# Kernel optimization log

Hardware: AMD Instinct MI355X
Metric: run time of the kernel (lower is better)

Reference implementation:

```python
import jax, jax.numpy as jnp
import numpy as np

B, N, D, E = 64, 128, 64, 131072  # graphs, nodes/graph, d_model, edges


def setup_inputs() -> dict:
    key = jax.random.key(0)
    ks = jax.random.split(key, 7)
    x = jax.random.normal(ks[0], (B * N, D), jnp.float32)
    # sorted batch assignment: exactly N nodes per graph
    batch = jnp.repeat(jnp.arange(B, dtype=jnp.int32), N)
    # intra-graph random edges
    eb = jax.random.randint(ks[1], (E,), 0, B)
    ls = jax.random.randint(ks[2], (E,), 0, N)
    ld = jax.random.randint(ks[3], (E,), 0, N)
    edge_index = jnp.stack([eb * N + ls, eb * N + ld], axis=0)
    edge_attr = jax.random.normal(ks[4], (E, D), jnp.float32)
    virtual_x_weight = jax.random.normal(ks[5], (1, D), jnp.float32) * 0.02
    virtual_edge_attr_weight = jax.random.normal(ks[6], (1, D), jnp.float32) * 0.02
    return {
        "x": x,
        "edge_attr": edge_attr,
        "virtual_x_weight": virtual_x_weight,
        "virtual_edge_attr_weight": virtual_edge_attr_weight,
        "batch": batch,
        "edge_index": edge_index,
        "num_graphs": B,
        "max_nodes": N,
    }


def reference(x, edge_attr, virtual_x_weight, virtual_edge_attr_weight,
              batch, edge_index, num_graphs, max_nodes):
    b, n = num_graphs, max_nodes
    total, d = x.shape
    # per-graph node counts and start offsets (to_dense_batch bookkeeping)
    counts = jax.ops.segment_sum(jnp.ones(total, jnp.int32), batch, num_segments=b)
    starts = jnp.cumsum(counts) - counts              # exclusive prefix sum
    pos = jnp.arange(total) - starts[batch]           # local node position in graph

    # to_dense_batch + virtual-node row 0 (scatter directly into padded tensor)
    x_with_vn = jnp.zeros((b, n + 1, d), x.dtype).at[batch, pos + 1].set(x)
    x_with_vn = x_with_vn.at[:, 0, :].set(virtual_x_weight[0])
    mask = jnp.zeros((b, n), bool).at[batch, pos].set(True)

    # to_dense_adj (duplicate edges sum) scattered directly at +1 offsets
    src, dst = edge_index[0], edge_index[1]
    eb = batch[src]
    ls = src - starts[eb] + 1
    ld = dst - starts[eb] + 1
    adj = jnp.zeros((b, n + 1, n + 1, d), edge_attr.dtype).at[eb, ls, ld].add(edge_attr)
    ve = virtual_edge_attr_weight[0]
    adj = adj.at[:, 0, 1:, :].set(ve)
    adj = adj.at[:, 1:, 0, :].set(ve)
    return x_with_vn, adj, mask
```

## Files before the change

### kernel.cpp

```cpp
#include <hip/hip_runtime.h>
#include <stdint.h>

#define NB 64
#define NN 128
#define ND 64
#define NE 131072
#define NP1 129

#define X_ELEMS   (NB * NP1 * ND)
#define ADJ_ELEMS (NB * NP1 * NP1 * ND)
#define MASK_ELEMS (NB * NN)
#define TOTAL_ELEMS (X_ELEMS + ADJ_ELEMS + MASK_ELEMS)

#define NCELLS (NB * NN * NN)
#define CNT_WORDS (NCELLS / 4)
#define WS_REQ ((size_t)CNT_WORDS * 4)


__global__ __launch_bounds__(256) void zero_cnt_kernel(unsigned int* __restrict__ cnt) {
  cnt[blockIdx.x * 256u + threadIdx.x] = 0u;
}

__global__ __launch_bounds__(256) void count_kernel(
    const int* __restrict__ ei, unsigned int* __restrict__ cnt) {
  unsigned int e = blockIdx.x * 256u + threadIdx.x;
  unsigned int src = (unsigned int)ei[e];
  unsigned int dst = (unsigned int)ei[NE + e];
  unsigned int cell = (src << 7) | (dst & 127u);
  atomicAdd(&cnt[cell >> 2], 1u << ((cell & 3u) << 3));
}

__global__ __launch_bounds__(256) void fill_kernel(
    const float* __restrict__ x, const float* __restrict__ vxw,
    const float* __restrict__ vew, float* __restrict__ out) {
  unsigned int base = (blockIdx.x * 256u + threadIdx.x) * 4u;
  float4 r;
  if (base < X_ELEMS) {
    unsigned int d = base & 63u;
    unsigned int rowflat = base >> 6;
    unsigned int row = rowflat % 129u;
    if (row == 0u) r = *(const float4*)(vxw + d);
    else r = *(const float4*)(x + ((((rowflat / 129u) << 7) + row - 1u) << 6) + d);
  } else if (base < X_ELEMS + ADJ_ELEMS) {
    unsigned int rel = base - X_ELEMS;
    unsigned int d = rel & 63u;
    unsigned int rc = rel >> 6;
    unsigned int col = rc % 129u;
    unsigned int row = (rc / 129u) % 129u;
    if ((row == 0u) != (col == 0u)) r = *(const float4*)(vew + d);
    else r = make_float4(0.f, 0.f, 0.f, 0.f);
  } else {
    r = make_float4(1.f, 1.f, 1.f, 1.f);
  }
  *(float4*)(out + base) = r;
}

template <int HYBRID>
__global__ __launch_bounds__(256) void scatter_kernel(
    const float* __restrict__ ea, const int* __restrict__ ei,
    const unsigned int* __restrict__ cnt, float* __restrict__ out) {
  unsigned int t = blockIdx.x * 256u + threadIdx.x;
  unsigned int e = t >> 6, lane = t & 63u;

  unsigned int src = (unsigned int)ei[e];
  unsigned int dst = (unsigned int)ei[NE + e];
  unsigned int eb = src >> 7;
  unsigned int ls = (src & 127u) + 1u;
  unsigned int ld = (dst & 127u) + 1u;
  unsigned int dstIdx = (unsigned int)X_ELEMS +
      (((eb * 129u + ls) * 129u + ld) << 6) + lane;
  float v = ea[(e << 6) + lane];

  if (HYBRID) {
    unsigned int cell = (src << 7) | (dst & 127u);
    unsigned int c = (cnt[cell >> 2] >> ((cell & 3u) << 3)) & 255u;
    if (c == 1u) { out[dstIdx] = v; return; }
  }
  atomicAdd(out + dstIdx, v);
}

extern "C" void kernel_launch(void* const* d_in, const int* in_sizes, int n_in,
                              void* d_out, int out_size, void* d_ws, size_t ws_size,
                              hipStream_t stream) {
  const float* x   = (const float*)d_in[0];
  const float* ea  = (const float*)d_in[1];
  const float* vxw = (const float*)d_in[2];
  const float* vew = (const float*)d_in[3];
  const int* ei = (const int*)d_in[5];
  float* out = (float*)d_out;

  if (ws_size >= WS_REQ) {
    unsigned int* cnt = (unsigned int*)d_ws;
    zero_cnt_kernel<<<CNT_WORDS / 256u, 256, 0, stream>>>(cnt);
    count_kernel<<<NE / 256u, 256, 0, stream>>>(ei, cnt);
    fill_kernel<<<TOTAL_ELEMS / 4u / 256u, 256, 0, stream>>>(x, vxw, vew, out);
    scatter_kernel<1><<<NE * 64u / 256u, 256, 0, stream>>>(ea, ei, cnt, out);
  } else {
    fill_kernel<<<TOTAL_ELEMS / 4u / 256u, 256, 0, stream>>>(x, vxw, vew, out);
    scatter_kernel<0><<<NE * 64u / 256u, 256, 0, stream>>>(ea, ei, nullptr, out);
  }
}
```

Baseline: 85.92 us.

## Replace fill-then-scatter with per-row edge lists gathered during dense build

Adds a binning pass that records each edge's id and destination column in a fixed-capacity per-source-row list alongside the per-cell counts. The dense adjacency is then built in a single pass: each nonzero cell scans its row list and sums the matching edge features, so the separate scatter pass and its second write over the output go away. The cost is a linear scan of up to 96 list entries per nonzero cell, plus random gather reads of edge features. Rows with more than 96 edges would be silently truncated.

Result: slower. 185.2 us (+115.5%).

```diff
diff --git a/kernel.cpp b/kernel.cpp
--- a/kernel.cpp
+++ b/kernel.cpp
@@ -14,20 +14,79 @@
 
 #define NCELLS (NB * NN * NN)
 #define CNT_WORDS (NCELLS / 4)
-#define WS_REQ ((size_t)CNT_WORDS * 4)
+#define NROWS (NB * NN)
+#define ROWCAP 96
+#define LIST_OFF_W (CNT_WORDS + NROWS)
+#define ZERO_WORDS (CNT_WORDS + NROWS)
+#define WS_WORDS (LIST_OFF_W + NROWS * ROWCAP)
+#define WS_REQ ((size_t)WS_WORDS * 4)
 
 
-__global__ __launch_bounds__(256) void zero_cnt_kernel(unsigned int* __restrict__ cnt) {
-  cnt[blockIdx.x * 256u + threadIdx.x] = 0u;
+__global__ __launch_bounds__(256) void zero_kernel(unsigned int* __restrict__ ws) {
+  ws[blockIdx.x * 256u + threadIdx.x] = 0u;
 }
 
-__global__ __launch_bounds__(256) void count_kernel(
-    const int* __restrict__ ei, unsigned int* __restrict__ cnt) {
+__global__ __launch_bounds__(256) void bin_kernel(
+    const int* __restrict__ ei, unsigned int* __restrict__ ws) {
   unsigned int e = blockIdx.x * 256u + threadIdx.x;
   unsigned int src = (unsigned int)ei[e];
   unsigned int dst = (unsigned int)ei[NE + e];
   unsigned int cell = (src << 7) | (dst & 127u);
-  atomicAdd(&cnt[cell >> 2], 1u << ((cell & 3u) << 3));
+  atomicAdd(&ws[cell >> 2], 1u << ((cell & 3u) << 3));
+  unsigned int idx = atomicAdd(&ws[CNT_WORDS + src], 1u);
+  if (idx < ROWCAP)
+    ws[LIST_OFF_W + src * ROWCAP + idx] = (e << 8) | ((dst & 127u) + 1u);
+}
+
+__global__ __launch_bounds__(256) void build_kernel(
+    const float* __restrict__ x, const float* __restrict__ vxw,
+    const float* __restrict__ vew, const float* __restrict__ ea,
+    const unsigned int* __restrict__ ws, float* __restrict__ out) {
+  unsigned int base = (blockIdx.x * 256u + threadIdx.x) * 4u;
+  float4 v;
+
+  if (base < X_ELEMS) {
+    unsigned int d = base & 63u;
+    unsigned int rowflat = base >> 6;
+    unsigned int row = rowflat % 129u;
+    if (row == 0u) v = *(const float4*)(vxw + d);
+    else v = *(const float4*)(x + ((((rowflat / 129u) << 7) + row - 1u) << 6) + d);
+  } else if (base < X_ELEMS + ADJ_ELEMS) {
+    unsigned int rel = base - X_ELEMS;
+    unsigned int d = rel & 63u;
+    unsigned int rc = rel >> 6;
+    unsigned int col = rc % 129u;
+    unsigned int t = rc / 129u;
+    unsigned int row = t % 129u;
+    unsigned int b = t / 129u;
+    if (row != 0u && col != 0u) {
+      unsigned int src  = (b << 7) + row - 1u;
+      unsigned int cell = (src << 7) | (col - 1u);
+      unsigned int n = (ws[cell >> 2] >> ((cell & 3u) << 3)) & 255u;
+      v = make_float4(0.f, 0.f, 0.f, 0.f);
+      if (n != 0u) {
+        unsigned int m = ws[CNT_WORDS + src]; if (m > ROWCAP) m = ROWCAP;
+        const unsigned int* lst = ws + LIST_OFF_W + src * ROWCAP;
+        unsigned int found = 0u;
+        for (unsigned int k = 0u; k < m; ++k) {
+          unsigned int u = lst[k];
+          if ((u & 255u) == col) {
+            const float4 a = *(const float4*)(ea + ((u >> 8) << 6) + d);
+            v.x += a.x; v.y += a.y; v.z += a.z; v.w += a.w;
+            if (++found == n) break;
+          }
+        }
+      }
+    } else if ((row == 0u) != (col == 0u)) {
+      v = *(const float4*)(vew + d);
+    } else {
+      v = make_float4(0.f, 0.f, 0.f, 0.f);
+    }
+  } else {
+    v = make_float4(1.f, 1.f, 1.f, 1.f);
+  }
+
+  *(float4*)(out + base) = v;
 }
 
 __global__ __launch_bounds__(256) void fill_kernel(
@@ -55,28 +114,18 @@
   *(float4*)(out + base) = r;
 }
 
-template <int HYBRID>
 __global__ __launch_bounds__(256) void scatter_kernel(
     const float* __restrict__ ea, const int* __restrict__ ei,
-    const unsigned int* __restrict__ cnt, float* __restrict__ out) {
+    float* __restrict__ out) {
   unsigned int t = blockIdx.x * 256u + threadIdx.x;
   unsigned int e = t >> 6, lane = t & 63u;
-
   unsigned int src = (unsigned int)ei[e];
   unsigned int dst = (unsigned int)ei[NE + e];
   unsigned int eb = src >> 7;
   unsigned int ls = (src & 127u) + 1u;
   unsigned int ld = (dst & 127u) + 1u;
-  unsigned int dstIdx = (unsigned int)X_ELEMS +
-      (((eb * 129u + ls) * 129u + ld) << 6) + lane;
-  float v = ea[(e << 6) + lane];
-
-  if (HYBRID) {
-    unsigned int cell = (src << 7) | (dst & 127u);
-    unsigned int c = (cnt[cell >> 2] >> ((cell & 3u) << 3)) & 255u;
-    if (c == 1u) { out[dstIdx] = v; return; }
-  }
-  atomicAdd(out + dstIdx, v);
+  atomicAdd(out + X_ELEMS + (((eb * 129u + ls) * 129u + ld) << 6) + lane,
+            ea[(e << 6) + lane]);
 }
 
 extern "C" void kernel_launch(void* const* d_in, const int* in_sizes, int n_in,
@@ -90,13 +139,13 @@
   float* out = (float*)d_out;
 
   if (ws_size >= WS_REQ) {
-    unsigned int* cnt = (unsigned int*)d_ws;
-    zero_cnt_kernel<<<CNT_WORDS / 256u, 256, 0, stream>>>(cnt);
-    count_kernel<<<NE / 256u, 256, 0, stream>>>(ei, cnt);
-    fill_kernel<<<TOTAL_ELEMS / 4u / 256u, 256, 0, stream>>>(x, vxw, vew, out);
-    scatter_kernel<1><<<NE * 64u / 256u, 256, 0, stream>>>(ea, ei, cnt, out);
+    unsigned int* ws = (unsigned int*)d_ws;
+    zero_kernel<<<ZERO_WORDS / 256u, 256, 0, stream>>>(ws);
+    bin_kernel<<<NE / 256u, 256, 0, stream>>>(ei, ws);
+    build_kernel<<<TOTAL_ELEMS / 4u / 256u, 256, 0, stream>>>(
+        x, vxw, vew, ea, ws, out);
   } else {
     fill_kernel<<<TOTAL_ELEMS / 4u / 256u, 256, 0, stream>>>(x, vxw, vew, out);
-    scatter_kernel<0><<<NE * 64u / 256u, 256, 0, stream>>>(ea, ei, nullptr, out);
+    scatter_kernel<<<NE * 64u / 256u, 256, 0, stream>>>(ea, ei, out);
   }
 }
```
